# Performance work log

Hardware: AMD Instinct MI355X
Metric: run time of the kernel (lower is better)

Reference implementation:

```python
import jax, jax.numpy as jnp
import numpy as np

L_SEG = 20   # number of CFT segments (hard-coded in original forward)
M_CHEB = 8   # Chebyshev quadrature order per segment


def _cft_magnitude(x, modes):
    """|CFT(x)| at integer frequencies [0, modes).

    Faithful to vectorized_batched_cft_decomposed with L=20, M=8, but only
    evaluated at the first `modes` frequencies (identical values; the original
    computes all rfft freqs then slices). Segment loop is folded into a single
    einsum by absorbing the per-segment phase shift into the quadrature weights.
    x: (B, C, N) real. Returns (B, C, modes) float.
    """
    n = x.shape[-1]
    t = jnp.linspace(0.0, 1.0, n)
    freqs = jnp.arange(modes, dtype=x.dtype)  # rfftfreq(n, d=1/n)[:modes]
    seg_len = 1.0 / L_SEG
    starts = jnp.linspace(0.0, 1.0, L_SEG + 1)[:-1]  # (L,)
    k = jnp.arange(M_CHEB, dtype=x.dtype)
    cheb = -jnp.cos((2.0 * k + 1.0) * jnp.pi / (2.0 * M_CHEB))  # (M,) nodes in [-1,1]
    T = jnp.cos(k[:, None] * jnp.arccos(cheb)[None, :])  # (K=M, M) Chebyshev T_k at nodes
    angle = cheb[:, None] * (freqs[None, :] * (2.0 * jnp.pi * seg_len / 2.0))  # (M, F)
    Wr = jnp.einsum('km,mf->kf', T, jnp.cos(angle)) * (seg_len / 2.0)  # (M, F)
    Wi = jnp.einsum('km,mf->kf', T, -jnp.sin(angle)) * (seg_len / 2.0)
    # piecewise-linear interpolation of x at the Chebyshev nodes of every segment
    t_seg = starts[:, None] + seg_len / 2.0 * (cheb + 1.0)[None, :]  # (L, M)
    right = jnp.clip(jnp.searchsorted(t, t_seg), 0, n - 1)
    left = jnp.clip(right - 1, 0, None)
    t_l, t_r = t[left], t[right]
    denom = jnp.where(t_r - t_l == 0.0, 1.0, t_r - t_l)
    w_r = (t_seg - t_l) / denom
    w_l = 1.0 - w_r
    seg = w_l * x[:, :, left] + w_r * x[:, :, right]  # (B, C, L, M)
    # per-segment phase shift exp(-i*2*pi*f*a) folded into combined weights
    phi = 2.0 * jnp.pi * starts[:, None] * freqs[None, :]  # (L, F)
    cs, sn = jnp.cos(phi), jnp.sin(phi)
    Ar = Wr[None] * cs[:, None, :] + Wi[None] * sn[:, None, :]   # (L, M, F)
    Ai = -Wr[None] * sn[:, None, :] + Wi[None] * cs[:, None, :]
    real = jnp.einsum('bclm,lmf->bcf', seg, Ar)
    imag = jnp.einsum('bclm,lmf->bcf', seg, Ai)
    return jnp.sqrt(real * real + imag * imag)


def setup_inputs() -> dict:
    key = jax.random.key(0)
    ks = jax.random.split(key, 4)
    B, Cin, Cout, N, modes = 32, 64, 64, 8192, 32
    scale = 1.0 / (Cin * Cout)
    return {
        'x': jax.random.normal(ks[0], (B, Cin, N), dtype=jnp.float32),
        'w1_real': scale * jax.random.uniform(ks[1], (Cin, Cout, modes), dtype=jnp.float32),
        'w1_imag': scale * jax.random.uniform(ks[2], (Cin, Cout, modes), dtype=jnp.float32),
        'gate_w': jax.random.normal(ks[3], (Cout, Cin), dtype=jnp.float32) / np.sqrt(Cin),
        'ln_gamma': jnp.ones((modes,), dtype=jnp.float32),
        'ln_beta': jnp.zeros((modes,), dtype=jnp.float32),
    }


def reference(x, w1_real, w1_imag, gate_w, ln_gamma, ln_beta):
    n = x.shape[-1]
    n_rfft = n // 2 + 1
    modes = w1_real.shape[-1]
    x_fft = jnp.fft.rfft(x)  # (B, C, n_rfft) complex64
    # CFT magnitude is detached in the original (x_cft.detach())
    mag = jax.lax.stop_gradient(_cft_magnitude(x, modes))  # (B, C, modes)
    # LayerNorm over the modes axis (eps = 1e-5, torch default)
    mu = jnp.mean(mag, axis=-1, keepdims=True)
    var = jnp.mean((mag - mu) ** 2, axis=-1, keepdims=True)
    g_norm = (mag - mu) / jnp.sqrt(var + 1e-5) * ln_gamma + ln_beta
    # 1x1 conv (no bias) over channels, then sigmoid gate
    gate = jax.nn.sigmoid(jnp.einsum('oi,bif->bof', gate_w, g_norm))  # (B, Cout, modes)
    gated = x_fft[:, :, :modes] * gate  # requires Cin == Cout
    w1 = w1_real + 1j * w1_imag  # (Cin, Cout, modes) complex
    out_modes = jnp.einsum('bix,iox->box', gated, w1)
    pad = jnp.zeros(out_modes.shape[:2] + (n_rfft - modes,), dtype=out_modes.dtype)
    out_ft = jnp.concatenate([out_modes, pad], axis=-1)
    return jnp.fft.irfft(out_ft, n=n)
```

## Files before the change

kernel.cpp:

```cpp
#include <hip/hip_runtime.h>
#include <hip/hip_bf16.h>
#include <math.h>

#define NN    8192
#define NROWS 2048
#define FF    32
#define LM    160

static constexpr int TRIG   = 0;
static constexpr int W1RT   = 524288;
static constexpr int W1IT   = 655360;
static constexpr int GWT    = 786432;
static constexpr int AR_    = 790528;
static constexpr int AI_    = 795648;
static constexpr int WL_    = 800768;
static constexpr int WR_    = 800928;
static constexpr int IL_    = 801088;
static constexpr int IR_    = 801248;
static constexpr int XR_    = 801408;
static constexpr int XI_    = 866944;
static constexpr int GN_    = 932480;
static constexpr int ARAI   = 998016;
static constexpr int TRIGT_ = 1129088;

#define PI_D 3.14159265358979323846

__global__ __launch_bounds__(256) void k_trig(float* __restrict__ ws) {
  int idx = blockIdx.x * 256 + threadIdx.x;
  int k4 = idx >> 8, f = (idx >> 2) & 63, j = idx & 3;
  int n = 4 * k4 + j;
  int fr = f & 31;
  int p = (fr * n) & (NN - 1);
  float ang = (float)p * (float)(2.0 * PI_D / (double)NN);
  float s, c;
  sincosf(ang, &s, &c);
  float v = (f < 32) ? c : s;
  ws[TRIG + idx] = v;
  ws[TRIGT_ + f * NN + n] = v;
}

__global__ __launch_bounds__(256) void k_cft_tables(float* __restrict__ ws) {
  int tid = blockIdx.x * 256 + threadIdx.x;
  if (tid >= LM * FF) return;
  int j = tid >> 5, f = tid & 31;
  int l = j >> 3, m = j & 7;
  double cheb[8];
  #pragma unroll
  for (int mm = 0; mm < 8; ++mm)
    cheb[mm] = -cos((2.0 * mm + 1.0) * PI_D / 16.0);

  double Wr = 0.0, Wi = 0.0;
  #pragma unroll
  for (int mm = 0; mm < 8; ++mm) {
    double T = cos((double)m * acos(cheb[mm]));
    double ang = cheb[mm] * (double)f * (PI_D * 0.05);
    Wr += T * cos(ang);
    Wi += T * (-sin(ang));
  }
  Wr *= 0.025; Wi *= 0.025;
  double phi = 2.0 * PI_D * ((double)l * 0.05) * (double)f;
  double cs = cos(phi), sn = sin(phi);
  ws[AR_ + j * FF + f] = (float)(Wr * cs + Wi * sn);
  ws[AI_ + j * FF + f] = (float)(-Wr * sn + Wi * cs);

  if (f == 0) {
    double v = (double)l * 0.05 + 0.025 * (cheb[m] + 1.0);
    int r = (int)(v * 8191.0);
    while ((double)r / 8191.0 < v) ++r;
    while (r > 0 && (double)(r - 1) / 8191.0 >= v) --r;
    if (r > 8191) r = 8191;
    int le = r - 1; if (le < 0) le = 0;
    double tl = (double)le / 8191.0, tr = (double)r / 8191.0;
    double den = (tr - tl == 0.0) ? 1.0 : (tr - tl);
    double wr = (v - tl) / den;
    ws[WL_ + j] = (float)(1.0 - wr);
    ws[WR_ + j] = (float)wr;
    ((int*)ws)[IL_ + j] = le;
    ((int*)ws)[IR_ + j] = r;
  }
}

__global__ __launch_bounds__(256) void k_transpose(const float* __restrict__ w1r,
                                                   const float* __restrict__ w1i,
                                                   const float* __restrict__ gw,
                                                   float* __restrict__ ws) {
  int idx = blockIdx.x * 256 + threadIdx.x;
  if (idx >= 32 * 64 * 64) return;
  int o = idx & 63, i = (idx >> 6) & 63, f = idx >> 12;
  ws[W1RT + (f * 64 + i) * 64 + o] = w1r[(i * 64 + o) * FF + f];
  ws[W1IT + (f * 64 + i) * 64 + o] = w1i[(i * 64 + o) * FF + f];
  if (idx < 4096) {
    ws[GWT + idx] = gw[(idx & 63) * 64 + (idx >> 6)];
  }
}

__global__ __launch_bounds__(256) void k_fwd_gemm(const float* __restrict__ x,
                                                  const float* __restrict__ ws,
                                                  float* __restrict__ part) {
  __shared__ __align__(16) float xs[64 * 128];
  const int rt = blockIdx.x >> 6, kc = blockIdx.x & 63;
  const int t = threadIdx.x;
  const int w = t >> 6, lane = t & 63;
  const int half = lane >> 5, fl = lane & 31;
  const int rblock = rt * 64;
  const float4* __restrict__ tg4 = (const float4*)(ws + TRIG);
  const int k40 = kc * 32;

  float4 tc = tg4[(size_t)k40 * 64 + fl];
  float4 tn = tg4[(size_t)k40 * 64 + 32 + fl];

  const int c4 = t & 31, r0 = t >> 5;
  const int kb = kc * 128;
  #pragma unroll
  for (int p = 0; p < 8; ++p) {
    int row = r0 + 8 * p;
    float4 v = *(const float4*)(x + (size_t)(rblock + row) * NN + kb + c4 * 4);
    *(float4*)(&xs[row * 128 + c4 * 4]) = v;
  }

  float accC[8], accS[8];
  #pragma unroll
  for (int r = 0; r < 8; ++r) { accC[r] = 0.f; accS[r] = 0.f; }

  __syncthreads();

  const float* __restrict__ xbase = &xs[(w * 16 + half * 8) * 128];

#define FWD_STEP(IT, TC, TS)                                                    \
  {                                                                             \
    _Pragma("unroll")                                                           \
    for (int j = 0; j < 8; ++j) {                                               \
      float4 xv = *(const float4*)(xbase + j * 128 + (IT) * 4);                 \
      accC[j] = fmaf(xv.w, (TC).w, fmaf(xv.z, (TC).z,                           \
                fmaf(xv.y, (TC).y, fmaf(xv.x, (TC).x, accC[j]))));              \
      accS[j] = fmaf(xv.w, (TS).w, fmaf(xv.z, (TS).z,                           \
                fmaf(xv.y, (TS).y, fmaf(xv.x, (TS).x, accS[j]))));              \
    }                                                                           \
  }

  #pragma unroll 4
  for (int it = 0; it < 31; ++it) {
    float4 tc2 = tg4[(size_t)(k40 + it + 1) * 64 + fl];
    float4 tn2 = tg4[(size_t)(k40 + it + 1) * 64 + 32 + fl];
    FWD_STEP(it, tc, tn);
    tc = tc2; tn = tn2;
  }
  FWD_STEP(31, tc, tn);
#undef FWD_STEP

  float* __restrict__ pp = part + ((size_t)kc * NROWS + rblock + w * 16 + half * 8) * 64;
  #pragma unroll
  for (int j = 0; j < 8; ++j) {
    pp[j * 64 + fl]      = accC[j];
    pp[j * 64 + 32 + fl] = accS[j];
  }
}

__global__ __launch_bounds__(256) void k_fred(const float* __restrict__ part,
                                              float* __restrict__ ws) {
  int idx = blockIdx.x * 256 + threadIdx.x;
  int row = idx >> 6, f = idx & 63;
  float s = 0.f;
  #pragma unroll 8
  for (int kc = 0; kc < 64; ++kc)
    s += part[((size_t)kc * NROWS + row) * 64 + f];
  if (f < 32) ws[XR_ + row * FF + f] = s;
  else        ws[XI_ + row * FF + (f - 32)] = -s;
}

__global__ __launch_bounds__(256) void k_cft(const float* __restrict__ x,
                                             const float* __restrict__ gamma,
                                             const float* __restrict__ beta,
                                             float* __restrict__ ws) {
  const int sub = threadIdx.x >> 6, li = threadIdx.x & 63;
  const int row = blockIdx.x * 4 + sub;
  const float* __restrict__ xr = x + (size_t)row * NN;
  __shared__ float seg[4][LM];
  #pragma unroll
  for (int g = 0; g < 3; ++g) {
    int j = li + 64 * g;
    if (j < LM) {
      int il = ((const int*)ws)[IL_ + j];
      int ir = ((const int*)ws)[IR_ + j];
      seg[sub][j] = ws[WL_ + j] * xr[il] + ws[WR_ + j] * xr[ir];
    }
  }
  __syncthreads();
  if (li < FF) {
    float re = 0.f, im = 0.f;
    #pragma unroll 8
    for (int j = 0; j < LM; ++j) {
      float sv = seg[sub][j];
      re = fmaf(sv, ws[AR_ + j * FF + li], re);
      im = fmaf(sv, ws[AI_ + j * FF + li], im);
    }
    float mag = sqrtf(re * re + im * im);
    float mu = mag;
    mu += __shfl_xor(mu, 1);  mu += __shfl_xor(mu, 2);  mu += __shfl_xor(mu, 4);
    mu += __shfl_xor(mu, 8);  mu += __shfl_xor(mu, 16);
    mu *= (1.0f / 32.0f);
    float d = mag - mu;
    float vv = d * d;
    vv += __shfl_xor(vv, 1);  vv += __shfl_xor(vv, 2);  vv += __shfl_xor(vv, 4);
    vv += __shfl_xor(vv, 8);  vv += __shfl_xor(vv, 16);
    vv *= (1.0f / 32.0f);
    float g = d / sqrtf(vv + 1e-5f) * gamma[li] + beta[li];
    ws[GN_ + row * FF + li] = g;
  }
}

__global__ __launch_bounds__(64) void k_gate(float* __restrict__ ws) {
  int bidx = blockIdx.x;
  int b = bidx >> 5, f = bidx & 31;
  int o = threadIdx.x;
  __shared__ float gn[64], gr[64], gi[64];
  int rowb = b * 64;
  gn[o] = ws[GN_ + (rowb + o) * FF + f];
  float xre = ws[XR_ + (rowb + o) * FF + f];
  float xim = ws[XI_ + (rowb + o) * FF + f];
  __syncthreads();
  float acc = 0.f;
  #pragma unroll 16
  for (int i = 0; i < 64; ++i)
    acc = fmaf(ws[GWT + i * 64 + o], gn[i], acc);
  float gate = 1.0f / (1.0f + expf(-acc));
  gr[o] = xre * gate;
  gi[o] = xim * gate;
  __syncthreads();
  float Yr = 0.f, Yi = 0.f;
  const float* __restrict__ w1rt = ws + W1RT + f * 4096;
  const float* __restrict__ w1it = ws + W1IT + f * 4096;
  #pragma unroll 8
  for (int i = 0; i < 64; ++i) {
    float a = gr[i], bb2 = gi[i];
    float wr = w1rt[i * 64 + o], wi = w1it[i * 64 + o];
    Yr = fmaf(a, wr, Yr); Yr = fmaf(-bb2, wi, Yr);
    Yi = fmaf(a, wi, Yi); Yi = fmaf(bb2, wr, Yi);
  }
  float* A = ws + ARAI + (size_t)(rowb + o) * 64;
  if (f == 0) {
    A[0]  = Yr * (1.0f / (float)NN);
    A[32] = 0.0f;
  } else {
    A[f]      = Yr * (2.0f / (float)NN);
    A[32 + f] = -Yi * (2.0f / (float)NN);
  }
}

__global__ __launch_bounds__(256) void k_inv(const float* __restrict__ ws,
                                             float* __restrict__ out) {
  __shared__ __align__(16) float As[32 * 64];
  const int blk = blockIdx.x;
  const int bb = blk >> 5, cc = blk & 31;
  const int t = threadIdx.x;
  const int w = t >> 6, lane = t & 63;
  const int rowbase = bb * 32;
  const float* __restrict__ trigt = ws + TRIGT_;
  const int colb = cc * 256 + lane * 4;

  float4 tg0 = *(const float4*)(trigt + (size_t)0 * NN + colb);
  float4 tg1 = *(const float4*)(trigt + (size_t)1 * NN + colb);
  float4 tg2 = *(const float4*)(trigt + (size_t)2 * NN + colb);
  float4 tg3 = *(const float4*)(trigt + (size_t)3 * NN + colb);

  #pragma unroll
  for (int p = 0; p < 2; ++p) {
    int idx = t + 256 * p;
    int r = idx >> 4, q = idx & 15;
    *(float4*)(&As[r * 64 + q * 4]) =
        *(const float4*)(ws + ARAI + (size_t)(rowbase + r) * 64 + q * 4);
  }

  float4 acc[8];
  #pragma unroll
  for (int r = 0; r < 8; ++r) acc[r] = make_float4(0.f, 0.f, 0.f, 0.f);

  __syncthreads();

#define INV_STEP(F0)                                                            \
  {                                                                             \
    _Pragma("unroll")                                                           \
    for (int r = 0; r < 8; ++r) {                                               \
      float4 av = *(const float4*)(&As[(w * 8 + r) * 64 + (F0)]);               \
      acc[r].x = fmaf(av.x, tg0.x, acc[r].x); acc[r].y = fmaf(av.x, tg0.y, acc[r].y); \
      acc[r].z = fmaf(av.x, tg0.z, acc[r].z); acc[r].w = fmaf(av.x, tg0.w, acc[r].w); \
      acc[r].x = fmaf(av.y, tg1.x, acc[r].x); acc[r].y = fmaf(av.y, tg1.y, acc[r].y); \
      acc[r].z = fmaf(av.y, tg1.z, acc[r].z); acc[r].w = fmaf(av.y, tg1.w, acc[r].w); \
      acc[r].x = fmaf(av.z, tg2.x, acc[r].x); acc[r].y = fmaf(av.z, tg2.y, acc[r].y); \
      acc[r].z = fmaf(av.z, tg2.z, acc[r].z); acc[r].w = fmaf(av.z, tg2.w, acc[r].w); \
      acc[r].x = fmaf(av.w, tg3.x, acc[r].x); acc[r].y = fmaf(av.w, tg3.y, acc[r].y); \
      acc[r].z = fmaf(av.w, tg3.z, acc[r].z); acc[r].w = fmaf(av.w, tg3.w, acc[r].w); \
    }                                                                           \
  }

  for (int fo = 0; fo < 15; ++fo) {
    int f0 = fo * 4;
    float4 n0 = *(const float4*)(trigt + (size_t)(f0 + 4) * NN + colb);
    float4 n1 = *(const float4*)(trigt + (size_t)(f0 + 5) * NN + colb);
    float4 n2 = *(const float4*)(trigt + (size_t)(f0 + 6) * NN + colb);
    float4 n3 = *(const float4*)(trigt + (size_t)(f0 + 7) * NN + colb);
    INV_STEP(f0);
    tg0 = n0; tg1 = n1; tg2 = n2; tg3 = n3;
  }
  INV_STEP(60);
#undef INV_STEP

  #pragma unroll
  for (int r = 0; r < 8; ++r) {
    int row = rowbase + w * 8 + r;
    *(float4*)(out + (size_t)row * NN + colb) = acc[r];
  }
}

extern "C" void kernel_launch(void* const* d_in, const int* in_sizes, int n_in,
                              void* d_out, int out_size, void* d_ws, size_t ws_size,
                              hipStream_t stream) {
  const float* x     = (const float*)d_in[0];
  const float* w1r   = (const float*)d_in[1];
  const float* w1i   = (const float*)d_in[2];
  const float* gw    = (const float*)d_in[3];
  const float* gamma = (const float*)d_in[4];
  const float* beta  = (const float*)d_in[5];
  float* out = (float*)d_out;
  float* ws = (float*)d_ws;
  float* part = (float*)d_out;

  hipLaunchKernelGGL(k_trig,       dim3(2048), dim3(256), 0, stream, ws);
  hipLaunchKernelGGL(k_cft_tables, dim3(20),   dim3(256), 0, stream, ws);
  hipLaunchKernelGGL(k_transpose,  dim3(512),  dim3(256), 0, stream, w1r, w1i, gw, ws);
  hipLaunchKernelGGL(k_fwd_gemm,   dim3(2048), dim3(256), 0, stream, x, ws, part);
  hipLaunchKernelGGL(k_fred,       dim3(512),  dim3(256), 0, stream, part, ws);
  hipLaunchKernelGGL(k_cft,        dim3(512),  dim3(256), 0, stream, x, gamma, beta, ws);
  hipLaunchKernelGGL(k_gate,       dim3(1024), dim3(64),  0, stream, ws);
  hipLaunchKernelGGL(k_inv,        dim3(2048), dim3(256), 0, stream, ws, out);
}
```

Measured before the change: 211.1 us.

## Double-buffer LDS reads in forward DFT GEMM, vectorize reduction, simplify CFT tables

The forward DFT GEMM now loads the next column of x from shared memory into a second register buffer while doing FMAs on the current one, and sets a minimum-occupancy launch bound. The partial-sum reduction kernel reads and writes float4 values with a quarter of the blocks. The CFT table kernel uses hardcoded Chebyshev nodes and a recurrence in place of cos/acos. These changes target LDS latency stalls and memory-instruction count, at the cost of higher register pressure in the GEMM.

```diff
diff --git a/kernel.cpp b/kernel.cpp
--- a/kernel.cpp
+++ b/kernel.cpp
@@ -44,16 +44,24 @@
   if (tid >= LM * FF) return;
   int j = tid >> 5, f = tid & 31;
   int l = j >> 3, m = j & 7;
-  double cheb[8];
-  #pragma unroll
-  for (int mm = 0; mm < 8; ++mm)
-    cheb[mm] = -cos((2.0 * mm + 1.0) * PI_D / 16.0);
+  const double cheb[8] = {
+    -0.98078528040323044913, -0.83146961230254523708,
+    -0.55557023301960222474, -0.19509032201612826785,
+     0.19509032201612826785,  0.55557023301960222474,
+     0.83146961230254523708,  0.98078528040323044913 };
 
   double Wr = 0.0, Wi = 0.0;
   #pragma unroll
   for (int mm = 0; mm < 8; ++mm) {
-    double T = cos((double)m * acos(cheb[mm]));
-    double ang = cheb[mm] * (double)f * (PI_D * 0.05);
+    double c = cheb[mm];
+    double T;
+    if (m == 0) T = 1.0;
+    else {
+      double a = 1.0, b = c;
+      for (int q = 1; q < m; ++q) { double t = 2.0 * c * b - a; a = b; b = t; }
+      T = b;
+    }
+    double ang = c * (double)f * (PI_D * 0.05);
     Wr += T * cos(ang);
     Wi += T * (-sin(ang));
   }
@@ -94,9 +102,9 @@
   }
 }
 
-__global__ __launch_bounds__(256) void k_fwd_gemm(const float* __restrict__ x,
-                                                  const float* __restrict__ ws,
-                                                  float* __restrict__ part) {
+__global__ __launch_bounds__(256, 4) void k_fwd_gemm(const float* __restrict__ x,
+                                                     const float* __restrict__ ws,
+                                                     float* __restrict__ part) {
   __shared__ __align__(16) float xs[64 * 128];
   const int rt = blockIdx.x >> 6, kc = blockIdx.x & 63;
   const int t = threadIdx.x;
@@ -106,9 +114,6 @@
   const float4* __restrict__ tg4 = (const float4*)(ws + TRIG);
   const int k40 = kc * 32;
 
-  float4 tc = tg4[(size_t)k40 * 64 + fl];
-  float4 tn = tg4[(size_t)k40 * 64 + 32 + fl];
-
   const int c4 = t & 31, r0 = t >> 5;
   const int kb = kc * 128;
   #pragma unroll
@@ -126,27 +131,47 @@
 
   const float* __restrict__ xbase = &xs[(w * 16 + half * 8) * 128];
 
-#define FWD_STEP(IT, TC, TS)                                                    \
+#define FWD_LOAD(DST, COL)                                                      \
+  {                                                                             \
+    _Pragma("unroll")                                                           \
+    for (int j = 0; j < 8; ++j)                                                 \
+      DST[j] = *(const float4*)(xbase + j * 128 + (COL) * 4);                   \
+  }
+
+#define FWD_FMA(XV, TC, TS)                                                     \
   {                                                                             \
     _Pragma("unroll")                                                           \
     for (int j = 0; j < 8; ++j) {                                               \
-      float4 xv = *(const float4*)(xbase + j * 128 + (IT) * 4);                 \
-      accC[j] = fmaf(xv.w, (TC).w, fmaf(xv.z, (TC).z,                           \
-                fmaf(xv.y, (TC).y, fmaf(xv.x, (TC).x, accC[j]))));              \
-      accS[j] = fmaf(xv.w, (TS).w, fmaf(xv.z, (TS).z,                           \
-                fmaf(xv.y, (TS).y, fmaf(xv.x, (TS).x, accS[j]))));              \
+      accC[j] = fmaf(XV[j].w, (TC).w, fmaf(XV[j].z, (TC).z,                     \
+                fmaf(XV[j].y, (TC).y, fmaf(XV[j].x, (TC).x, accC[j]))));        \
+      accS[j] = fmaf(XV[j].w, (TS).w, fmaf(XV[j].z, (TS).z,                     \
+                fmaf(XV[j].y, (TS).y, fmaf(XV[j].x, (TS).x, accS[j]))));        \
     }                                                                           \
   }
 
-  #pragma unroll 4
-  for (int it = 0; it < 31; ++it) {
-    float4 tc2 = tg4[(size_t)(k40 + it + 1) * 64 + fl];
-    float4 tn2 = tg4[(size_t)(k40 + it + 1) * 64 + 32 + fl];
-    FWD_STEP(it, tc, tn);
-    tc = tc2; tn = tn2;
-  }
-  FWD_STEP(31, tc, tn);
-#undef FWD_STEP
+  float4 xva[8], xvb[8];
+  float4 tc = tg4[(size_t)k40 * 64 + fl];
+  float4 tn = tg4[(size_t)k40 * 64 + 32 + fl];
+  FWD_LOAD(xva, 0);
+
+  for (int it = 0; it < 30; it += 2) {
+    float4 tcB = tg4[(size_t)(k40 + it + 1) * 64 + fl];
+    float4 tnB = tg4[(size_t)(k40 + it + 1) * 64 + 32 + fl];
+    FWD_LOAD(xvb, it + 1);
+    FWD_FMA(xva, tc, tn);
+    float4 tcA = tg4[(size_t)(k40 + it + 2) * 64 + fl];
+    float4 tnA = tg4[(size_t)(k40 + it + 2) * 64 + 32 + fl];
+    FWD_LOAD(xva, it + 2);
+    FWD_FMA(xvb, tcB, tnB);
+    tc = tcA; tn = tnA;
+  }
+  float4 tcL = tg4[(size_t)(k40 + 31) * 64 + fl];
+  float4 tnL = tg4[(size_t)(k40 + 31) * 64 + 32 + fl];
+  FWD_LOAD(xvb, 31);
+  FWD_FMA(xva, tc, tn);
+  FWD_FMA(xvb, tcL, tnL);
+#undef FWD_LOAD
+#undef FWD_FMA
 
   float* __restrict__ pp = part + ((size_t)kc * NROWS + rblock + w * 16 + half * 8) * 64;
   #pragma unroll
@@ -159,13 +184,20 @@
 __global__ __launch_bounds__(256) void k_fred(const float* __restrict__ part,
                                               float* __restrict__ ws) {
   int idx = blockIdx.x * 256 + threadIdx.x;
-  int row = idx >> 6, f = idx & 63;
-  float s = 0.f;
-  #pragma unroll 8
-  for (int kc = 0; kc < 64; ++kc)
-    s += part[((size_t)kc * NROWS + row) * 64 + f];
-  if (f < 32) ws[XR_ + row * FF + f] = s;
-  else        ws[XI_ + row * FF + (f - 32)] = -s;
+  int row = idx >> 4, fq = idx & 15;
+  const float4* __restrict__ p4 = (const float4*)part;
+  float4 s = make_float4(0.f, 0.f, 0.f, 0.f);
+  #pragma unroll 16
+  for (int kc = 0; kc < 64; ++kc) {
+    float4 v = p4[((size_t)kc * NROWS + row) * 16 + fq];
+    s.x += v.x; s.y += v.y; s.z += v.z; s.w += v.w;
+  }
+  if (fq < 8) {
+    *(float4*)(ws + XR_ + row * FF + fq * 4) = s;
+  } else {
+    float4 n = make_float4(-s.x, -s.y, -s.z, -s.w);
+    *(float4*)(ws + XI_ + row * FF + (fq - 8) * 4) = n;
+  }
 }
 
 __global__ __launch_bounds__(256) void k_cft(const float* __restrict__ x,
@@ -329,7 +361,7 @@
   hipLaunchKernelGGL(k_cft_tables, dim3(20),   dim3(256), 0, stream, ws);
   hipLaunchKernelGGL(k_transpose,  dim3(512),  dim3(256), 0, stream, w1r, w1i, gw, ws);
   hipLaunchKernelGGL(k_fwd_gemm,   dim3(2048), dim3(256), 0, stream, x, ws, part);
-  hipLaunchKernelGGL(k_fred,       dim3(512),  dim3(256), 0, stream, part, ws);
+  hipLaunchKernelGGL(k_fred,       dim3(128),  dim3(256), 0, stream, part, ws);
   hipLaunchKernelGGL(k_cft,        dim3(512),  dim3(256), 0, stream, x, gamma, beta, ws);
   hipLaunchKernelGGL(k_gate,       dim3(1024), dim3(64),  0, stream, ws);
   hipLaunchKernelGGL(k_inv,        dim3(2048), dim3(256), 0, stream, ws, out);
```

New measurement: 212.2 us. Within noise of the previous version (+0.5%).
